# Kernel tuning notes

Hardware: AMD Instinct MI355X
Metric: run time of the kernel (lower is better)

Reference implementation:

```python
import jax, jax.numpy as jnp
import numpy as np

NUM_HEADS = 12
HEAD_DIM = 64
HIDDEN = NUM_HEADS * HEAD_DIM  # 768


def setup_inputs() -> dict:
    key = jax.random.key(0)
    ks = jax.random.split(key, 18)
    B, Ni, Nt, H = 8, 1024, 512, HIDDEN
    inp = {
        "hidden_states": jax.random.normal(ks[0], (B, Ni, H), jnp.float32),
        "text": jax.random.normal(ks[1], (B, Nt, H), jnp.float32),
    }
    names = ["Wq", "Wk", "Wv", "Wqt", "Wkt", "Wvt", "Wo"]
    for i, n in enumerate(names):
        inp[n] = jax.random.normal(ks[2 + i], (H, H), jnp.float32) * 0.02
        inp["b" + n[1:]] = jnp.zeros((H,), jnp.float32)
    return inp


def _split_heads(x):
    # [B, S, H] -> [B, h, S, dh]
    B, S, _ = x.shape
    return x.reshape(B, S, NUM_HEADS, HEAD_DIM).transpose(0, 2, 1, 3)


def _merge_heads(x):
    # [B, h, S, dh] -> [B, S, H]
    B, h, S, dh = x.shape
    return x.transpose(0, 2, 1, 3).reshape(B, S, h * dh)


def _attend(q, k, v):
    scale = 1.0 / jnp.sqrt(jnp.asarray(HEAD_DIM, q.dtype))
    scores = jnp.einsum("bhqd,bhkd->bhqk", q, k) * scale
    probs = jax.nn.softmax(scores, axis=-1)
    ctx = jnp.einsum("bhqk,bhkd->bhqd", probs, v)
    return ctx, probs


def reference(hidden_states, text, Wq, bq, Wk, bk, Wv, bv,
              Wqt, bqt, Wkt, bkt, Wvt, bvt, Wo, bo):
    q_i = _split_heads(hidden_states @ Wq + bq)
    k_i = _split_heads(hidden_states @ Wk + bk)
    v_i = _split_heads(hidden_states @ Wv + bv)
    q_t = _split_heads(text @ Wqt + bqt)
    k_t = _split_heads(text @ Wkt + bkt)
    v_t = _split_heads(text @ Wvt + bvt)

    ctx_ii, weights = _attend(q_i, k_i, v_i)   # img -> img (weights returned, vis=True)
    ctx_tt, _ = _attend(q_t, k_t, v_t)         # text -> text
    ctx_it, _ = _attend(q_i, k_t, v_t)         # img queries, text keys/values
    ctx_ti, _ = _attend(q_t, k_i, v_i)         # text queries, img keys/values

    out_img = (_merge_heads(ctx_ii) + _merge_heads(ctx_it)) * 0.5 @ Wo + bo
    out_text = (_merge_heads(ctx_tt) + _merge_heads(ctx_ti)) * 0.5 @ Wo + bo
    return out_img, out_text, weights
```

## Files before the change

### kernel.cpp

```cpp
#include <hip/hip_runtime.h>

typedef __attribute__((ext_vector_type(4))) float f32x4;
typedef __attribute__((ext_vector_type(8))) short short8;
typedef __attribute__((ext_vector_type(4))) short s16x4;
typedef __attribute__((ext_vector_type(4))) unsigned short us4;
typedef unsigned short u16;
typedef unsigned char uchar;

__device__ __forceinline__ u16 f2b(float f) {
  union { float f; unsigned u; } a; a.f = f;
  unsigned r = a.u + 0x7fffu + ((a.u >> 16) & 1u);
  return (u16)(r >> 16);
}
__device__ __forceinline__ unsigned cvtpk2(float lo, float hi) {
  unsigned r;
  asm("v_cvt_pk_bf16_f32 %0, %1, %2" : "=v"(r) : "v"(lo), "v"(hi));
  return r;
}
__device__ __forceinline__ short8 cvt8(f32x4 a, f32x4 b) {
  union { unsigned u[4]; short8 s; } r;
  r.u[0] = cvtpk2(a[0], a[1]); r.u[1] = cvtpk2(a[2], a[3]);
  r.u[2] = cvtpk2(b[0], b[1]); r.u[3] = cvtpk2(b[2], b[3]);
  return r.s;
}
#define SWZ(r, byteoff) ((((r) * 128) + (byteoff)) ^ (((r) & 7) << 4))

typedef __attribute__((address_space(1))) const void* gp1;
typedef __attribute__((address_space(3))) void* lp3;
__device__ __forceinline__ void gload16(const void* g, void* lds_wave_uniform_base) {
  __builtin_amdgcn_global_load_lds((gp1)g, (lp3)lds_wave_uniform_base, 16, 0, 0);
}
__device__ __forceinline__ void waitv0() { asm volatile("s_waitcnt vmcnt(0)" ::: "memory"); }
__device__ __forceinline__ void waitv1() { asm volatile("s_waitcnt vmcnt(1)" ::: "memory"); }
__device__ __forceinline__ void waitv2() { asm volatile("s_waitcnt vmcnt(2)" ::: "memory"); }
__device__ __forceinline__ void abar()  { __builtin_amdgcn_s_barrier(); }
__device__ __forceinline__ void sbar()  { __builtin_amdgcn_sched_barrier(0); }

__global__ __launch_bounds__(256) void prep_kernel(
    const float* w0, const float* w1, const float* w2, const float* w3,
    const float* w4, const float* w5, const float* w6, u16* wt,
    const float* __restrict__ h, const float* __restrict__ tx, u16* __restrict__ xb)
{
  const int bid = blockIdx.x, t = threadIdx.x;
  if (bid < 1008) {
    __shared__ float tile[64][65];
    const float* Ws[7] = {w0, w1, w2, w3, w4, w5, w6};
    int z = bid / 144, rem = bid % 144;
    const float* W = Ws[z];
    u16* out = wt + (size_t)z * 589824;
    const int r0 = (rem / 12) * 64, c0 = (rem % 12) * 64;
#pragma unroll
    for (int i = 0; i < 4; ++i) {
      int idx = i * 256 + t;
      int r = idx >> 4, c = (idx & 15) * 4;
      f32x4 v = *(const f32x4*)(W + (size_t)(r0 + r) * 768 + (c0 + c));
      tile[r][c + 0] = v[0]; tile[r][c + 1] = v[1];
      tile[r][c + 2] = v[2]; tile[r][c + 3] = v[3];
    }
    __syncthreads();
#pragma unroll
    for (int i = 0; i < 4; ++i) {
      int idx = i * 256 + t;
      int rn = idx >> 4, c = (idx & 15) * 4;
      union { us4 o; unsigned u[2]; } o;
      o.u[0] = cvtpk2(tile[c + 0][rn], tile[c + 1][rn]);
      o.u[1] = cvtpk2(tile[c + 2][rn], tile[c + 3][rn]);
      *(us4*)(out + (size_t)(c0 + rn) * 768 + (r0 + c)) = o.o;
    }
  } else {
    size_t e = ((size_t)(bid - 1008) * 256 + t) * 8;
    const float* src; size_t off;
    if (e < 6291456) { src = h; off = e; } else { src = tx; off = e - 6291456; }
    f32x4 v0 = *(const f32x4*)(src + off), v1 = *(const f32x4*)(src + off + 4);
    *(short8*)(xb + e) = cvt8(v0, v1);
  }
}

__global__ __launch_bounds__(256) void proj_kernel(
    const u16* __restrict__ Xb, const u16* __restrict__ wt,
    const float* __restrict__ bq, const float* __restrict__ bk, const float* __restrict__ bv,
    const float* __restrict__ bqt, const float* __restrict__ bkt, const float* __restrict__ bvt,
    u16* __restrict__ qi, u16* __restrict__ ki, u16* __restrict__ vti,
    u16* __restrict__ qt, u16* __restrict__ ktx, u16* __restrict__ vtt)
{
  const int bid = blockIdx.x;
  const int wk = (bid & 7) * 216 + (bid >> 3);
  const bool img = wk < 1152;
  const int id = img ? wk : wk - 1152;
  const int y = img ? (id >> 6) : (id >> 5);
  const int x = img ? (id & 63) : (id & 31);
  const int z = y / 6, n0 = (y % 6) * 128, m0 = x * 128;
  const int S = img ? 1024 : 512, logS = img ? 10 : 9;
  const u16* X = img ? Xb : Xb + 6291456;
  const u16* Wt = wt + (img ? 0 : (size_t)3 * 589824) + (size_t)y * 98304;
  const float* bias = img ? (z == 0 ? bq : z == 1 ? bk : bv)
                          : (z == 0 ? bqt : z == 1 ? bkt : bvt);
  u16* out = img ? (z == 0 ? qi : z == 1 ? ki : vti)
                 : (z == 0 ? qt : z == 1 ? ktx : vtt);
  const bool vmode = (z == 2);
  __shared__ unsigned char sm[36864];
  unsigned char* Asm = sm;
  unsigned char* Bsm = sm + 16384;
  const int t = threadIdx.x, w = t >> 6, l = t & 63;
  const int wm = (w & 1) * 64, wn = (w >> 1) * 64;
  f32x4 acc[4][4] = {};
  for (int k0 = 0; k0 < 768; k0 += 64) {
#pragma unroll
    for (int j = 0; j < 4; ++j) {
      int chunk = j * 4 + w;
      int r = chunk * 8 + (l >> 3);
      int cb = ((l & 7) * 16) ^ ((r & 7) << 4);
      gload16(X + (size_t)(m0 + r) * 768 + k0 + cb / 2, Asm + chunk * 1024);
    }
#pragma unroll
    for (int j = 0; j < 4; ++j) {
      int chunk = j * 4 + w;
      int r = chunk * 8 + (l >> 3);
      int cb = ((l & 7) * 16) ^ ((r & 7) << 4);
      gload16(Wt + (size_t)r * 768 + k0 + cb / 2, Bsm + chunk * 1024);
    }
    __syncthreads();
#pragma unroll
    for (int kc = 0; kc < 2; ++kc) {
      short8 af[4], bfr[4];
      const int koff = (kc * 32 + (l >> 4) * 8) * 2;
#pragma unroll
      for (int ms = 0; ms < 4; ++ms) {
        int row = wm + ms * 16 + (l & 15);
        af[ms] = *(const short8*)(Asm + SWZ(row, koff));
      }
#pragma unroll
      for (int ns = 0; ns < 4; ++ns) {
        int row = wn + ns * 16 + (l & 15);
        bfr[ns] = *(const short8*)(Bsm + SWZ(row, koff));
      }
      __builtin_amdgcn_s_setprio(1);
#pragma unroll
      for (int ms = 0; ms < 4; ++ms)
#pragma unroll
        for (int ns = 0; ns < 4; ++ns)
          acc[ms][ns] = __builtin_amdgcn_mfma_f32_16x16x32_bf16(af[ms], bfr[ns], acc[ms][ns], 0, 0, 0);
      __builtin_amdgcn_s_setprio(0);
    }
    __syncthreads();
  }
  float bvv[4];
#pragma unroll
  for (int ns = 0; ns < 4; ++ns) bvv[ns] = bias[n0 + wn + ns * 16 + (l & 15)];
#pragma unroll
  for (int ms = 0; ms < 4; ++ms)
#pragma unroll
    for (int ns = 0; ns < 4; ++ns)
#pragma unroll
      for (int i = 0; i < 4; ++i) {
        u16 u = f2b(acc[ms][ns][i] + bvv[ns]);
        int mm = wm + ms * 16 + (l >> 4) * 4 + i;
        int nn = wn + ns * 16 + (l & 15);
        int row = vmode ? nn : mm, col = vmode ? mm : nn;
        *(u16*)(sm + row * 272 + col * 2) = u;
      }
  __syncthreads();
  if (!vmode) {
#pragma unroll
    for (int i = 0; i < 8; ++i) {
      int idx = i * 256 + t;
      int r = idx >> 4, c = (idx & 15) * 8;
      short8 v = *(const short8*)(sm + r * 272 + c * 2);
      int sg = m0 + r, b = sg >> logS, s = sg & (S - 1);
      int n = n0 + c, hh = n >> 6, d = n & 63;
      *(short8*)(out + (((size_t)b * 12 + hh) * S + s) * 64 + d) = v;
    }
  } else {
#pragma unroll
    for (int i = 0; i < 8; ++i) {
      int idx = i * 256 + t;
      int r = idx >> 4, c = (idx & 15) * 8;
      short8 v = *(const short8*)(sm + r * 272 + c * 2);
      int n = n0 + r, hh = n >> 6, d = n & 63;
      int sg = m0 + c, b = sg >> logS, s = sg & (S - 1);
      *(short8*)(out + (((size_t)b * 12 + hh) * 64 + d) * S + s) = v;
    }
  }
}

__device__ __forceinline__ void stage_k8(const u16* Kp, int kt, uchar* Ksm, int w, int l) {
  int r = w * 8 + (l >> 3);
  int cb = ((l & 7) * 16) ^ ((r & 7) << 4);
  gload16(Kp + (size_t)(kt * 64 + r) * 64 + cb / 2, Ksm + w * 1024);
}
__device__ __forceinline__ void stage_v8(const u16* Vp, int kt, int Sk, uchar* Vsm, int w, int l) {
  int r = w * 8 + (l >> 3);
  int cb = ((l & 7) * 16) ^ ((r & 7) << 4);
  gload16(Vp + (size_t)r * Sk + kt * 64 + cb / 2, Vsm + w * 1024);
}
__device__ __forceinline__ void kfrags(const uchar* Ksm, int l, short8 kf[8]) {
#pragma unroll
  for (int kc = 0; kc < 2; ++kc)
#pragma unroll
    for (int sub = 0; sub < 4; ++sub) {
      int row = sub * 16 + (l & 15);
      kf[kc * 4 + sub] = *(const short8*)(Ksm + SWZ(row, (kc * 32 + (l >> 4) * 8) * 2));
    }
}
__device__ __forceinline__ void qk_swapped(const short8 qf[2], const short8 kf[8], f32x4 sfr[4]) {
  __builtin_amdgcn_s_setprio(1);
#pragma unroll
  for (int kc = 0; kc < 2; ++kc)
#pragma unroll
    for (int sub = 0; sub < 4; ++sub)
      sfr[sub] = __builtin_amdgcn_mfma_f32_16x16x32_bf16(kf[kc * 4 + sub], qf[kc], sfr[sub], 0, 0, 0);
  __builtin_amdgcn_s_setprio(0);
}
__device__ __forceinline__ void vfrags_sigma(const uchar* Vsm, int l, short8 vb[8]) {
#pragma unroll
  for (int kc = 0; kc < 2; ++kc)
#pragma unroll
    for (int ds = 0; ds < 4; ++ds) {
      int row = ds * 16 + (l & 15);
      union { s16x4 h[2]; short8 s; } u;
      u.h[0] = *(const s16x4*)(Vsm + SWZ(row, 64 * kc + 8 * (l >> 4)));
      u.h[1] = *(const s16x4*)(Vsm + SWZ(row, 64 * kc + 32 + 8 * (l >> 4)));
      vb[kc * 4 + ds] = u.s;
    }
}
__device__ __forceinline__ void pa_sigma(const float ps[16], short8 pa[2]) {
#pragma unroll
  for (int kc = 0; kc < 2; ++kc) {
    union { unsigned u[4]; short8 s; } r;
    r.u[0] = cvtpk2(ps[8 * kc + 0], ps[8 * kc + 1]);
    r.u[1] = cvtpk2(ps[8 * kc + 2], ps[8 * kc + 3]);
    r.u[2] = cvtpk2(ps[8 * kc + 4], ps[8 * kc + 5]);
    r.u[3] = cvtpk2(ps[8 * kc + 6], ps[8 * kc + 7]);
    pa[kc] = r.s;
  }
}
__device__ __forceinline__ void pv_sigma(const short8 pa[2], const short8 vb[8], f32x4 og[4]) {
  __builtin_amdgcn_s_setprio(1);
#pragma unroll
  for (int kc = 0; kc < 2; ++kc)
#pragma unroll
    for (int ds = 0; ds < 4; ++ds)
      og[ds] = __builtin_amdgcn_mfma_f32_16x16x32_bf16(pa[kc], vb[kc * 4 + ds], og[ds], 0, 0, 0);
  __builtin_amdgcn_s_setprio(0);
}
__device__ __forceinline__ void pass_unnorm(
    const u16* __restrict__ Kp, const u16* __restrict__ Vp, int Sk,
    const short8 qf[2], uchar* Ks0, uchar* Ks1, uchar* Vs0, uchar* Vs1,
    int w, int l, f32x4 og[4], float& ll)
{
  const int nkt = Sk >> 6;
  stage_k8(Kp, 0, Ks0, w, l);
  stage_v8(Vp, 0, Sk, Vs0, w, l);
  for (int kt = 0; kt < nkt; ++kt) {
    uchar* Kc = (kt & 1) ? Ks1 : Ks0;
    uchar* Vc = (kt & 1) ? Vs1 : Vs0;
    if (kt + 1 < nkt) {
      stage_k8(Kp, kt + 1, (kt & 1) ? Ks0 : Ks1, w, l);
      stage_v8(Vp, kt + 1, Sk, (kt & 1) ? Vs0 : Vs1, w, l);
      waitv2();
    } else {
      waitv0();
    }
    abar(); sbar();
    short8 kf[8];
    kfrags(Kc, l, kf);
    f32x4 sfr[4] = {};
    qk_swapped(qf, kf, sfr);
    float ps[16];
#pragma unroll
    for (int sub = 0; sub < 4; ++sub)
#pragma unroll
      for (int i = 0; i < 4; ++i) {
        float p = __expf(sfr[sub][i] * 0.125f);
        ll += p;
        ps[sub * 4 + i] = p;
      }
    short8 pa[2];
    pa_sigma(ps, pa);
    short8 vb[8];
    vfrags_sigma(Vc, l, vb);
    pv_sigma(pa, vb, og);
    sbar(); abar();
  }
}

__global__ __launch_bounds__(512, 4) void attn_kernel(
    const u16* __restrict__ qi, const u16* __restrict__ ki, const u16* __restrict__ vti,
    const u16* __restrict__ qt, const u16* __restrict__ ktx, const u16* __restrict__ vtt,
    u16* __restrict__ cimg, u16* __restrict__ ctxt, float* __restrict__ weights)
{
  __shared__ uchar smem[32768];
  const int t = threadIdx.x, w = t >> 6, l = t & 63;
  uchar* Ks0 = smem;
  uchar* Ks1 = smem + 8192;
  uchar* Vs0 = smem + 16384;
  uchar* Vs1 = smem + 24576;

  const int bid = blockIdx.x;
  const int wk = (bid & 7) * 144 + (bid >> 3);
  const bool img = wk < 768;
  const int id = img ? wk : wk - 768;
  const int x = img ? (id & 7) : (id & 3);
  const int head = img ? (id >> 3) : (id >> 2);
  const int b = head / 12, h = head % 12;
  const int Sq = img ? 1024 : 512;
  const int SkA = img ? 1024 : 512, SkB = img ? 512 : 1024;
  const u16* Qp = (img ? qi : qt) + (size_t)head * Sq * 64;
  const u16* KpA = (img ? ki : ktx) + (size_t)head * SkA * 64;
  const u16* VpA = (img ? vti : vtt) + (size_t)head * 64 * SkA;
  const u16* KpB = (img ? ktx : ki) + (size_t)head * SkB * 64;
  const u16* VpB = (img ? vtt : vti) + (size_t)head * 64 * SkB;
  u16* CTX = img ? cimg : ctxt;
  float* PROBS = img ? weights : nullptr;
  const int q0 = x * 128;
  const int qrow = q0 + w * 16 + (l & 15);

  short8 qf[2];
  qf[0] = *(const short8*)(Qp + (size_t)qrow * 64 + (l >> 4) * 8);
  qf[1] = *(const short8*)(Qp + (size_t)qrow * 64 + 32 + (l >> 4) * 8);

  f32x4 of[4] = {};
  if (PROBS) {
    float ll = 0.f;
    const int nkt = SkA >> 6;
    stage_k8(KpA, 0, Ks0, w, l);
    for (int kt = 0; kt < nkt; ++kt) {
      uchar* Kc = (kt & 1) ? Ks1 : Ks0;
      if (kt + 1 < nkt) {
        stage_k8(KpA, kt + 1, (kt & 1) ? Ks0 : Ks1, w, l);
        waitv1();
      } else {
        waitv0();
      }
      abar(); sbar();
      short8 kf[8];
      kfrags(Kc, l, kf);
      f32x4 sfr[4] = {};
      qk_swapped(qf, kf, sfr);
#pragma unroll
      for (int sub = 0; sub < 4; ++sub)
#pragma unroll
        for (int i = 0; i < 4; ++i) ll += __expf(sfr[sub][i] * 0.125f);
      sbar(); abar();
    }
    stage_k8(KpA, 0, Ks0, w, l);
    stage_v8(VpA, 0, SkA, Vs0, w, l);
    ll += __shfl_xor(ll, 16);
    ll += __shfl_xor(ll, 32);
    float rl = 1.0f / ll;
    float* prow = PROBS + ((size_t)head * Sq + qrow) * SkA;
    for (int kt = 0; kt < nkt; ++kt) {
      uchar* Kc = (kt & 1) ? Ks1 : Ks0;
      uchar* Vc = (kt & 1) ? Vs1 : Vs0;
      if (kt + 1 < nkt) {
        stage_k8(KpA, kt + 1, (kt & 1) ? Ks0 : Ks1, w, l);
        stage_v8(VpA, kt + 1, SkA, (kt & 1) ? Vs0 : Vs1, w, l);
        waitv2();
      } else {
        waitv0();
      }
      abar(); sbar();
      short8 kf[8];
      kfrags(Kc, l, kf);
      f32x4 sfr[4] = {};
      qk_swapped(qf, kf, sfr);
      float ps[16];
#pragma unroll
      for (int sub = 0; sub < 4; ++sub) {
#pragma unroll
        for (int i = 0; i < 4; ++i)
          ps[sub * 4 + i] = __expf(sfr[sub][i] * 0.125f) * rl;
        *(f32x4*)(prow + kt * 64 + sub * 16 + (l >> 4) * 4) = *(const f32x4*)&ps[sub * 4];
      }
      short8 pa[2];
      pa_sigma(ps, pa);
      short8 vb[8];
      vfrags_sigma(Vc, l, vb);
      pv_sigma(pa, vb, of);
      sbar(); abar();
    }
#pragma unroll
    for (int ds = 0; ds < 4; ++ds) of[ds] *= 0.5f;
  } else {
    float ll = 0.f;
    pass_unnorm(KpA, VpA, SkA, qf, Ks0, Ks1, Vs0, Vs1, w, l, of, ll);
    ll += __shfl_xor(ll, 16);
    ll += __shfl_xor(ll, 32);
    float r = 0.5f / ll;
#pragma unroll
    for (int i = 0; i < 4; ++i) {
      float lv = __int_as_float(__builtin_amdgcn_ds_bpermute(
          ((l >> 4) * 4 + i) * 4, __float_as_int(r)));
#pragma unroll
      for (int ds = 0; ds < 4; ++ds) of[ds][i] *= lv;
    }
  }
  {
    f32x4 og[4] = {};
    float l2 = 0.f;
    pass_unnorm(KpB, VpB, SkB, qf, Ks0, Ks1, Vs0, Vs1, w, l, og, l2);
    l2 += __shfl_xor(l2, 16);
    l2 += __shfl_xor(l2, 32);
    float r = 0.5f / l2;
#pragma unroll
    for (int i = 0; i < 4; ++i) {
      float lv = __int_as_float(__builtin_amdgcn_ds_bpermute(
          ((l >> 4) * 4 + i) * 4, __float_as_int(r)));
#pragma unroll
      for (int ds = 0; ds < 4; ++ds) of[ds][i] += og[ds][i] * lv;
    }
  }
  __syncthreads();
  {
    uchar* Wb = smem + w * 2176;
#pragma unroll
    for (int ds = 0; ds < 4; ++ds)
#pragma unroll
      for (int i = 0; i < 4; ++i)
        *(u16*)(Wb + ((l >> 4) * 4 + i) * 136 + (16 * ds + (l & 15)) * 2) = f2b(of[ds][i]);
#pragma unroll
    for (int i = 0; i < 2; ++i) {
      int it = i * 64 + l;
      int r = it >> 3, cg = it & 7;
      short8 v = *(const short8*)(Wb + r * 136 + cg * 16);
      int s = q0 + w * 16 + r;
      *(short8*)(CTX + ((size_t)b * Sq + s) * 768 + h * 64 + cg * 8) = v;
    }
  }
}

__global__ __launch_bounds__(256) void outproj_kernel(
    const u16* __restrict__ cimg, const u16* __restrict__ ctxt,
    const u16* __restrict__ Wto, const float* __restrict__ bias,
    float* __restrict__ out_img, float* __restrict__ out_text)
{
  const int bid = blockIdx.x;
  const int wk = (bid & 7) * 72 + (bid >> 3);
  const bool img = wk < 384;
  const int id = img ? wk : wk - 384;
  const int y = img ? (id >> 6) : (id >> 5);
  const int x = img ? (id & 63) : (id & 31);
  const u16* C = img ? cimg : ctxt;
  float* OUT = img ? out_img : out_text;
  const int m0 = x * 128, n0 = y * 128;
  __shared__ unsigned char sm[32768];
  unsigned char* Asm = sm;
  unsigned char* Bsm = sm + 16384;
  const int t = threadIdx.x, w = t >> 6, l = t & 63;
  const int wm = (w & 1) * 64, wn = (w >> 1) * 64;
  f32x4 acc[4][4] = {};
  for (int k0 = 0; k0 < 768; k0 += 64) {
#pragma unroll
    for (int j = 0; j < 4; ++j) {
      int chunk = j * 4 + w;
      int r = chunk * 8 + (l >> 3);
      int cb = ((l & 7) * 16) ^ ((r & 7) << 4);
      gload16(C + (size_t)(m0 + r) * 768 + k0 + cb / 2, Asm + chunk * 1024);
    }
#pragma unroll
    for (int j = 0; j < 4; ++j) {
      int chunk = j * 4 + w;
      int r = chunk * 8 + (l >> 3);
      int cb = ((l & 7) * 16) ^ ((r & 7) << 4);
      gload16(Wto + (size_t)(n0 + r) * 768 + k0 + cb / 2, Bsm + chunk * 1024);
    }
    __syncthreads();
#pragma unroll
    for (int kc = 0; kc < 2; ++kc) {
      short8 af[4], bfr[4];
      const int koff = (kc * 32 + (l >> 4) * 8) * 2;
#pragma unroll
      for (int ms = 0; ms < 4; ++ms) {
        int row = wm + ms * 16 + (l & 15);
        af[ms] = *(const short8*)(Asm + SWZ(row, koff));
      }
#pragma unroll
      for (int ns = 0; ns < 4; ++ns) {
        int row = wn + ns * 16 + (l & 15);
        bfr[ns] = *(const short8*)(Bsm + SWZ(row, koff));
      }
      __builtin_amdgcn_s_setprio(1);
#pragma unroll
      for (int ms = 0; ms < 4; ++ms)
#pragma unroll
        for (int ns = 0; ns < 4; ++ns)
          acc[ms][ns] = __builtin_amdgcn_mfma_f32_16x16x32_bf16(af[ms], bfr[ns], acc[ms][ns], 0, 0, 0);
      __builtin_amdgcn_s_setprio(0);
    }
    __syncthreads();
  }
#pragma unroll
  for (int ms = 0; ms < 4; ++ms)
#pragma unroll
    for (int ns = 0; ns < 4; ++ns) {
      float bv = bias[n0 + wn + ns * 16 + (l & 15)];
#pragma unroll
      for (int i = 0; i < 4; ++i) {
        int mm = m0 + wm + ms * 16 + (l >> 4) * 4 + i;
        int nn = n0 + wn + ns * 16 + (l & 15);
        OUT[(size_t)mm * 768 + nn] = acc[ms][ns][i] + bv;
      }
    }
}

extern "C" void kernel_launch(void* const* d_in, const int* in_sizes, int n_in,
                              void* d_out, int out_size, void* d_ws, size_t ws_size,
                              hipStream_t stream)
{
  const float* hidden = (const float*)d_in[0];
  const float* text   = (const float*)d_in[1];
  const float* Wq  = (const float*)d_in[2];  const float* bq  = (const float*)d_in[3];
  const float* Wk  = (const float*)d_in[4];  const float* bk  = (const float*)d_in[5];
  const float* Wv  = (const float*)d_in[6];  const float* bv  = (const float*)d_in[7];
  const float* Wqt = (const float*)d_in[8];  const float* bqt = (const float*)d_in[9];
  const float* Wkt = (const float*)d_in[10]; const float* bkt = (const float*)d_in[11];
  const float* Wvt = (const float*)d_in[12]; const float* bvt = (const float*)d_in[13];
  const float* Wo  = (const float*)d_in[14]; const float* bo  = (const float*)d_in[15];

  u16* wt   = (u16*)d_ws;
  u16* xb   = wt + 7 * 589824;
  u16* qi   = xb + 9437184;
  u16* ki   = qi + 6291456;
  u16* vti  = ki + 6291456;
  u16* qt   = vti + 6291456;
  u16* ktx  = qt + 3145728;
  u16* vtt  = ktx + 3145728;
  u16* cimg = vtt + 3145728;
  u16* ctxt = cimg + 6291456;

  float* out_img  = (float*)d_out;
  float* out_text = out_img + 6291456;
  float* weights  = out_text + 3145728;

  prep_kernel<<<5616, 256, 0, stream>>>(Wq, Wk, Wv, Wqt, Wkt, Wvt, Wo, wt,
                                        hidden, text, xb);
  proj_kernel<<<1728, 256, 0, stream>>>(xb, wt, bq, bk, bv, bqt, bkt, bvt,
                                        qi, ki, vti, qt, ktx, vtt);
  attn_kernel<<<1152, 512, 0, stream>>>(qi, ki, vti, qt, ktx, vtt,
                                        cimg, ctxt, weights);
  outproj_kernel<<<576, 256, 0, stream>>>(cimg, ctxt, wt + 6 * 589824, bo,
                                          out_img, out_text);
}
```

Before: 313.8 us.

## Double key tile to 128 per barrier stage and use exp2 with folded scale

Each pipeline stage now stages 128 keys of K and V into LDS instead of 64, halving the number of barrier and wait rounds per pass, with V in a new 256-byte-row swizzle. It also replaces expf with exp2f using a pre-folded scale, and folds the softmax normalisation into the exponent as a subtracted log2 instead of a multiply. LDS use doubles to 64 KiB per block, which may reduce how many blocks fit per CU and so lower occupancy.

```diff
diff --git a/kernel.cpp b/kernel.cpp
--- a/kernel.cpp
+++ b/kernel.cpp
@@ -24,6 +24,8 @@
   return r.s;
 }
 #define SWZ(r, byteoff) ((((r) * 128) + (byteoff)) ^ (((r) & 7) << 4))
+#define VSWZ(r, byteoff) (((r) * 256) + (((byteoff)) ^ (((r) & 15) << 4)))
+#define C2 0.18033688011112158f
 
 typedef __attribute__((address_space(1))) const void* gp1;
 typedef __attribute__((address_space(3))) void* lp3;
@@ -31,8 +33,8 @@
   __builtin_amdgcn_global_load_lds((gp1)g, (lp3)lds_wave_uniform_base, 16, 0, 0);
 }
 __device__ __forceinline__ void waitv0() { asm volatile("s_waitcnt vmcnt(0)" ::: "memory"); }
-__device__ __forceinline__ void waitv1() { asm volatile("s_waitcnt vmcnt(1)" ::: "memory"); }
 __device__ __forceinline__ void waitv2() { asm volatile("s_waitcnt vmcnt(2)" ::: "memory"); }
+__device__ __forceinline__ void waitv4() { asm volatile("s_waitcnt vmcnt(4)" ::: "memory"); }
 __device__ __forceinline__ void abar()  { __builtin_amdgcn_s_barrier(); }
 __device__ __forceinline__ void sbar()  { __builtin_amdgcn_sched_barrier(0); }
 
@@ -183,22 +185,30 @@
   }
 }
 
-__device__ __forceinline__ void stage_k8(const u16* Kp, int kt, uchar* Ksm, int w, int l) {
-  int r = w * 8 + (l >> 3);
-  int cb = ((l & 7) * 16) ^ ((r & 7) << 4);
-  gload16(Kp + (size_t)(kt * 64 + r) * 64 + cb / 2, Ksm + w * 1024);
-}
-__device__ __forceinline__ void stage_v8(const u16* Vp, int kt, int Sk, uchar* Vsm, int w, int l) {
-  int r = w * 8 + (l >> 3);
-  int cb = ((l & 7) * 16) ^ ((r & 7) << 4);
-  gload16(Vp + (size_t)r * Sk + kt * 64 + cb / 2, Vsm + w * 1024);
-}
-__device__ __forceinline__ void kfrags(const uchar* Ksm, int l, short8 kf[8]) {
+__device__ __forceinline__ void stage_k128(const u16* Kp, int kt, uchar* Ksm, int w, int l) {
+#pragma unroll
+  for (int call = 0; call < 2; ++call) {
+    int idx = call * 512 + w * 64 + l;
+    int r = idx >> 3, c16 = idx & 7;
+    int cb = (c16 * 16) ^ ((r & 7) << 4);
+    gload16(Kp + (size_t)(kt * 128 + r) * 64 + cb / 2, Ksm + call * 8192 + w * 1024);
+  }
+}
+__device__ __forceinline__ void stage_v128(const u16* Vp, int kt, int Sk, uchar* Vsm, int w, int l) {
+#pragma unroll
+  for (int call = 0; call < 2; ++call) {
+    int idx = call * 512 + w * 64 + l;
+    int r = idx >> 4, c16 = idx & 15;
+    int cb = (c16 * 16) ^ ((r & 15) << 4);
+    gload16(Vp + (size_t)r * Sk + kt * 128 + cb / 2, Vsm + call * 8192 + w * 1024);
+  }
+}
+__device__ __forceinline__ void kfrags(const uchar* Ksm, int ks, int l, short8 kf[8]) {
 #pragma unroll
   for (int kc = 0; kc < 2; ++kc)
 #pragma unroll
     for (int sub = 0; sub < 4; ++sub) {
-      int row = sub * 16 + (l & 15);
+      int row = ks * 64 + sub * 16 + (l & 15);
       kf[kc * 4 + sub] = *(const short8*)(Ksm + SWZ(row, (kc * 32 + (l >> 4) * 8) * 2));
     }
 }
@@ -211,15 +221,16 @@
       sfr[sub] = __builtin_amdgcn_mfma_f32_16x16x32_bf16(kf[kc * 4 + sub], qf[kc], sfr[sub], 0, 0, 0);
   __builtin_amdgcn_s_setprio(0);
 }
-__device__ __forceinline__ void vfrags_sigma(const uchar* Vsm, int l, short8 vb[8]) {
+__device__ __forceinline__ void vfrags_sigma(const uchar* Vsm, int ks, int l, short8 vb[8]) {
 #pragma unroll
   for (int kc = 0; kc < 2; ++kc)
 #pragma unroll
     for (int ds = 0; ds < 4; ++ds) {
       int row = ds * 16 + (l & 15);
+      int off0 = 128 * ks + 64 * kc + 8 * (l >> 4);
       union { s16x4 h[2]; short8 s; } u;
-      u.h[0] = *(const s16x4*)(Vsm + SWZ(row, 64 * kc + 8 * (l >> 4)));
-      u.h[1] = *(const s16x4*)(Vsm + SWZ(row, 64 * kc + 32 + 8 * (l >> 4)));
+      u.h[0] = *(const s16x4*)(Vsm + VSWZ(row, off0));
+      u.h[1] = *(const s16x4*)(Vsm + VSWZ(row, off0 + 32));
       vb[kc * 4 + ds] = u.s;
     }
 }
@@ -243,43 +254,48 @@
       og[ds] = __builtin_amdgcn_mfma_f32_16x16x32_bf16(pa[kc], vb[kc * 4 + ds], og[ds], 0, 0, 0);
   __builtin_amdgcn_s_setprio(0);
 }
+__device__ __forceinline__ void half_unnorm(const uchar* Kc, const uchar* Vc, int ks,
+                                            const short8 qf[2], int l, f32x4 og[4], float& ll) {
+  short8 kf[8];
+  kfrags(Kc, ks, l, kf);
+  f32x4 sfr[4] = {};
+  qk_swapped(qf, kf, sfr);
+  float ps[16];
+#pragma unroll
+  for (int sub = 0; sub < 4; ++sub)
+#pragma unroll
+    for (int i = 0; i < 4; ++i) {
+      float p = exp2f(sfr[sub][i] * C2);
+      ll += p;
+      ps[sub * 4 + i] = p;
+    }
+  short8 pa[2];
+  pa_sigma(ps, pa);
+  short8 vb[8];
+  vfrags_sigma(Vc, ks, l, vb);
+  pv_sigma(pa, vb, og);
+}
 __device__ __forceinline__ void pass_unnorm(
     const u16* __restrict__ Kp, const u16* __restrict__ Vp, int Sk,
     const short8 qf[2], uchar* Ks0, uchar* Ks1, uchar* Vs0, uchar* Vs1,
     int w, int l, f32x4 og[4], float& ll)
 {
-  const int nkt = Sk >> 6;
-  stage_k8(Kp, 0, Ks0, w, l);
-  stage_v8(Vp, 0, Sk, Vs0, w, l);
+  const int nkt = Sk >> 7;
+  stage_k128(Kp, 0, Ks0, w, l);
+  stage_v128(Vp, 0, Sk, Vs0, w, l);
   for (int kt = 0; kt < nkt; ++kt) {
     uchar* Kc = (kt & 1) ? Ks1 : Ks0;
     uchar* Vc = (kt & 1) ? Vs1 : Vs0;
     if (kt + 1 < nkt) {
-      stage_k8(Kp, kt + 1, (kt & 1) ? Ks0 : Ks1, w, l);
-      stage_v8(Vp, kt + 1, Sk, (kt & 1) ? Vs0 : Vs1, w, l);
-      waitv2();
+      stage_k128(Kp, kt + 1, (kt & 1) ? Ks0 : Ks1, w, l);
+      stage_v128(Vp, kt + 1, Sk, (kt & 1) ? Vs0 : Vs1, w, l);
+      waitv4();
     } else {
       waitv0();
     }
     abar(); sbar();
-    short8 kf[8];
-    kfrags(Kc, l, kf);
-    f32x4 sfr[4] = {};
-    qk_swapped(qf, kf, sfr);
-    float ps[16];
-#pragma unroll
-    for (int sub = 0; sub < 4; ++sub)
-#pragma unroll
-      for (int i = 0; i < 4; ++i) {
-        float p = __expf(sfr[sub][i] * 0.125f);
-        ll += p;
-        ps[sub * 4 + i] = p;
-      }
-    short8 pa[2];
-    pa_sigma(ps, pa);
-    short8 vb[8];
-    vfrags_sigma(Vc, l, vb);
-    pv_sigma(pa, vb, og);
+    half_unnorm(Kc, Vc, 0, qf, l, og, ll);
+    half_unnorm(Kc, Vc, 1, qf, l, og, ll);
     sbar(); abar();
   }
 }
@@ -289,12 +305,12 @@
     const u16* __restrict__ qt, const u16* __restrict__ ktx, const u16* __restrict__ vtt,
     u16* __restrict__ cimg, u16* __restrict__ ctxt, float* __restrict__ weights)
 {
-  __shared__ uchar smem[32768];
+  __shared__ uchar smem[65536];
   const int t = threadIdx.x, w = t >> 6, l = t & 63;
   uchar* Ks0 = smem;
-  uchar* Ks1 = smem + 8192;
-  uchar* Vs0 = smem + 16384;
-  uchar* Vs1 = smem + 24576;
+  uchar* Ks1 = smem + 16384;
+  uchar* Vs0 = smem + 32768;
+  uchar* Vs1 = smem + 49152;
 
   const int bid = blockIdx.x;
   const int wk = (bid & 7) * 144 + (bid >> 3);
@@ -322,61 +338,68 @@
   f32x4 of[4] = {};
   if (PROBS) {
     float ll = 0.f;
-    const int nkt = SkA >> 6;
-    stage_k8(KpA, 0, Ks0, w, l);
+    const int nkt = SkA >> 7;
+    stage_k128(KpA, 0, Ks0, w, l);
     for (int kt = 0; kt < nkt; ++kt) {
       uchar* Kc = (kt & 1) ? Ks1 : Ks0;
       if (kt + 1 < nkt) {
-        stage_k8(KpA, kt + 1, (kt & 1) ? Ks0 : Ks1, w, l);
-        waitv1();
+        stage_k128(KpA, kt + 1, (kt & 1) ? Ks0 : Ks1, w, l);
+        waitv2();
       } else {
         waitv0();
       }
       abar(); sbar();
-      short8 kf[8];
-      kfrags(Kc, l, kf);
-      f32x4 sfr[4] = {};
-      qk_swapped(qf, kf, sfr);
-#pragma unroll
-      for (int sub = 0; sub < 4; ++sub)
-#pragma unroll
-        for (int i = 0; i < 4; ++i) ll += __expf(sfr[sub][i] * 0.125f);
+#pragma unroll
+      for (int ks = 0; ks < 2; ++ks) {
+        short8 kf[8];
+        kfrags(Kc, ks, l, kf);
+        f32x4 sfr[4] = {};
+        qk_swapped(qf, kf, sfr);
+#pragma unroll
+        for (int sub = 0; sub < 4; ++sub)
+#pragma unroll
+          for (int i = 0; i < 4; ++i) ll += exp2f(sfr[sub][i] * C2);
+      }
       sbar(); abar();
     }
-    stage_k8(KpA, 0, Ks0, w, l);
-    stage_v8(VpA, 0, SkA, Vs0, w, l);
+    stage_k128(KpA, 0, Ks0, w, l);
+    stage_v128(VpA, 0, SkA, Vs0, w, l);
     ll += __shfl_xor(ll, 16);
     ll += __shfl_xor(ll, 32);
-    float rl = 1.0f / ll;
+    const float lb = -__log2f(ll);
     float* prow = PROBS + ((size_t)head * Sq + qrow) * SkA;
     for (int kt = 0; kt < nkt; ++kt) {
       uchar* Kc = (kt & 1) ? Ks1 : Ks0;
       uchar* Vc = (kt & 1) ? Vs1 : Vs0;
       if (kt + 1 < nkt) {
-        stage_k8(KpA, kt + 1, (kt & 1) ? Ks0 : Ks1, w, l);
-        stage_v8(VpA, kt + 1, SkA, (kt & 1) ? Vs0 : Vs1, w, l);
-        waitv2();
+        stage_k128(KpA, kt + 1, (kt & 1) ? Ks0 : Ks1, w, l);
+        stage_v128(VpA, kt + 1, SkA, (kt & 1) ? Vs0 : Vs1, w, l);
+        waitv4();
       } else {
         waitv0();
       }
       abar(); sbar();
-      short8 kf[8];
-      kfrags(Kc, l, kf);
-      f32x4 sfr[4] = {};
-      qk_swapped(qf, kf, sfr);
-      float ps[16];
-#pragma unroll
-      for (int sub = 0; sub < 4; ++sub) {
-#pragma unroll
-        for (int i = 0; i < 4; ++i)
-          ps[sub * 4 + i] = __expf(sfr[sub][i] * 0.125f) * rl;
-        *(f32x4*)(prow + kt * 64 + sub * 16 + (l >> 4) * 4) = *(const f32x4*)&ps[sub * 4];
-      }
-      short8 pa[2];
-      pa_sigma(ps, pa);
-      short8 vb[8];
-      vfrags_sigma(Vc, l, vb);
-      pv_sigma(pa, vb, of);
+#pragma unroll
+      for (int ks = 0; ks < 2; ++ks) {
+        short8 kf[8];
+        kfrags(Kc, ks, l, kf);
+        f32x4 sfr[4] = {};
+        qk_swapped(qf, kf, sfr);
+        float ps[16];
+#pragma unroll
+        for (int sub = 0; sub < 4; ++sub) {
+#pragma unroll
+          for (int i = 0; i < 4; ++i)
+            ps[sub * 4 + i] = exp2f(sfr[sub][i] * C2 + lb);
+          *(f32x4*)(prow + kt * 128 + ks * 64 + sub * 16 + (l >> 4) * 4) =
+              *(const f32x4*)&ps[sub * 4];
+        }
+        short8 pa[2];
+        pa_sigma(ps, pa);
+        short8 vb[8];
+        vfrags_sigma(Vc, ks, l, vb);
+        pv_sigma(pa, vb, of);
+      }
       sbar(); abar();
     }
 #pragma unroll
```

New measurement: 340.9 us. +8.6%, slower.
